# Optimization experiments

Hardware: AMD Instinct MI355X
Metric: run time of the kernel (lower is better)

The kernel has to match this reference:

```python
import jax, jax.numpy as jnp
import numpy as np

ATOM_VOC = 128
PAD = 0

def setup_inputs() -> dict:
    key = jax.random.key(0)
    ks = jax.random.split(key, 12)
    b, l, d_model, nhead, apo = 8, 256, 512, 16, 128
    atoms = jax.random.randint(ks[0], (b, l), 0, ATOM_VOC)
    chirals = jax.random.randint(ks[1], (b, l), 0, 4)
    coordinates = jax.random.normal(ks[2], (b, l, 3), dtype=jnp.float32)
    bonds = jax.random.randint(ks[3], (b, l, l), 0, 32)
    atype_emb = jax.random.normal(ks[4], (ATOM_VOC, d_model), jnp.float32).at[PAD].set(0.0)
    chiral_emb = jax.random.normal(ks[5], (4, d_model), jnp.float32).at[PAD].set(0.0)
    apair_w_tab = jax.random.normal(ks[6], (ATOM_VOC * ATOM_VOC, apo), jnp.float32)
    apair_b_tab = jax.random.normal(ks[7], (ATOM_VOC * ATOM_VOC, apo), jnp.float32)
    means = jnp.zeros((apo,), jnp.float32)
    stds = jnp.ones((apo,), jnp.float32)
    bond_emb = jax.random.normal(ks[8], (32, nhead), jnp.float32).at[PAD].set(0.0)
    lin_w = jax.random.normal(ks[9], (apo, nhead), jnp.float32) / np.sqrt(apo)
    lin_b = jax.random.normal(ks[10], (nhead,), jnp.float32)
    return dict(atoms=atoms, chirals=chirals, coordinates=coordinates, bonds=bonds,
                atype_emb=atype_emb, chiral_emb=chiral_emb, apair_w_tab=apair_w_tab,
                apair_b_tab=apair_b_tab, means=means, stds=stds, bond_emb=bond_emb,
                lin_w=lin_w, lin_b=lin_b)

def _safe_dist(coordinates):
    # pairwise distances [b,l,l]; safe-sqrt so grad at 0 distance is 0 (diagonal)
    diff = coordinates[:, None, :, :] - coordinates[:, :, None, :]
    s = jnp.sum(diff * diff, axis=-1)
    return jnp.where(s > 0, jnp.sqrt(jnp.where(s > 0, s, 1.0)), 0.0)

def reference(atoms, chirals, coordinates, bonds, atype_emb, chiral_emb,
              apair_w_tab, apair_b_tab, means, stds, bond_emb, lin_w, lin_b):
    # atoms_emb: [l, b, d_model]
    atoms_emb = (atype_emb[atoms] + chiral_emb[chirals]).transpose(1, 0, 2)
    dist = _safe_dist(coordinates)                      # [b,l,l]
    pair_idx = atoms[:, None, :] * ATOM_VOC + atoms[:, :, None]  # [b,l,l]
    ap = apair_w_tab[pair_idx] * dist[..., None] + apair_b_tab[pair_idx]  # [b,l,l,apo]
    std = jnp.abs(stds) + 1e-5
    gauss = jnp.exp(-0.5 * ((ap - means) / std) ** 2) / (np.sqrt(2.0 * np.pi) * std)
    apairs = jnp.einsum('bijk,kh->bijh', gauss, lin_w) + lin_b + bond_emb[bonds]
    pad_mask = (atoms == PAD)[:, None, :, None]         # mask over key/column dim
    apairs = jnp.where(pad_mask, -jnp.inf, apairs)
    return atoms_emb, apairs.transpose(0, 3, 1, 2)      # [b,nhead,l,l]
```

## Files before the change

kernel.cpp:

```cpp
#include <hip/hip_runtime.h>
#include <hip/hip_fp16.h>
#include <math.h>
#include <stdint.h>

#define B 8
#define L 256
#define DM 512
#define NH 16
#define APO 128
#define VOC 128
#define EMB (L * B * DM)

typedef __attribute__((ext_vector_type(8))) _Float16 half8v;
typedef __attribute__((ext_vector_type(4))) float float4v;

#define WSB_BOFF   1024
#define ORD_BOFF   9216
#define PACK_BOFF  24576
#define PACK_BYTES (128 * 128 * 256)
#define WS_NEED    ((size_t)PACK_BOFF + (size_t)PACK_BYTES)

__device__ __forceinline__ void g2lds16(const void* g, void* l) {
    __builtin_amdgcn_global_load_lds(
        (const __attribute__((address_space(1))) unsigned int*)g,
        (__attribute__((address_space(3))) unsigned int*)l, 16, 0, 0);
}

__global__ __launch_bounds__(256) void pack_kernel(const float* __restrict__ wtab,
                                                   const float* __restrict__ btab,
                                                   const float* __restrict__ means,
                                                   const float* __restrict__ stds,
                                                   const float* __restrict__ lin_w,
                                                   const int* __restrict__ atoms,
                                                   float* __restrict__ ws) {
    const float beta = sqrtf(0.5f * 1.4426950408889634f);
    const float gscale = 0.3989422804014327f;
    int t = threadIdx.x;

    if (blockIdx.x == 0) {
        unsigned short* wsB = (unsigned short*)((char*)ws + WSB_BOFF);
        for (int idx = t; idx < 4 * 64 * 8; idx += 256) {
            int p = idx >> 9;
            int lane = (idx >> 3) & 63;
            int e = idx & 7;
            int k = p * 32 + ((lane >> 4) << 3) + e;
            int h = lane & 15;
            float sigma = fabsf(stds[k]) + 1e-5f;
            float v = lin_w[k * NH + h] * (gscale / sigma);
            __half hv = __float2half(v);
            wsB[idx] = *reinterpret_cast<unsigned short*>(&hv);
        }
        __shared__ int hist[128];
        if (t < 128) hist[t] = 0;
        __syncthreads();
        for (int vb = t; vb < 2048; vb += 256)
            atomicAdd(&hist[atoms[vb] & 127], 1);
        __syncthreads();
        __shared__ int offs[128];
        if (t == 0) {
            int acc = 0;
            for (int bkt = 0; bkt < 128; ++bkt) { offs[bkt] = acc; acc += hist[bkt]; }
        }
        __syncthreads();
        int* order = (int*)((char*)ws + ORD_BOFF);
        for (int vb = t; vb < 2048; vb += 256) {
            int a = atoms[vb] & 127;
            int pos = atomicAdd(&offs[a], 1);
            order[pos] = vb;
        }
    }

    int idx = blockIdx.x * 256 + t;
    int r = idx >> 4;
    int a_i = r >> 7, a_j = r & 127;
    int U = idx & 15;
    int k0 = U * 8;
    size_t src = ((size_t)a_j * VOC + a_i) * APO + k0;
    const float4* w4p = (const float4*)(wtab + src);
    const float4* b4p = (const float4*)(btab + src);
    float4 w0 = w4p[0], w1 = w4p[1], b0 = b4p[0], b1 = b4p[1];
    float wq[8], bq[8];
    #pragma unroll
    for (int e = 0; e < 8; ++e) {
        int k = k0 + e;
        float sigma = fabsf(stds[k]) + 1e-5f;
        float ia = beta / sigma;
        float wvv = ((e < 4) ? ((const float*)&w0)[e] : ((const float*)&w1)[e - 4]) * ia;
        float bvv = (((e < 4) ? ((const float*)&b0)[e] : ((const float*)&b1)[e - 4])
                     - means[k]) * ia;
        wq[e] = wvv; bq[e] = bvv;
    }
    int wlo = 0, whi = 0, blo = 0, bhi = 0;
    wlo = __builtin_amdgcn_cvt_pk_fp8_f32(wq[0], wq[1], wlo, 0);
    wlo = __builtin_amdgcn_cvt_pk_fp8_f32(wq[2], wq[3], wlo, 1);
    whi = __builtin_amdgcn_cvt_pk_fp8_f32(wq[4], wq[5], whi, 0);
    whi = __builtin_amdgcn_cvt_pk_fp8_f32(wq[6], wq[7], whi, 1);
    blo = __builtin_amdgcn_cvt_pk_fp8_f32(bq[0], bq[1], blo, 0);
    blo = __builtin_amdgcn_cvt_pk_fp8_f32(bq[2], bq[3], blo, 1);
    bhi = __builtin_amdgcn_cvt_pk_fp8_f32(bq[4], bq[5], bhi, 0);
    bhi = __builtin_amdgcn_cvt_pk_fp8_f32(bq[6], bq[7], bhi, 1);
    int pu = U ^ (a_j & 15);
    uint4 o;
    o.x = (unsigned)wlo; o.y = (unsigned)whi;
    o.z = (unsigned)blo; o.w = (unsigned)bhi;
    *(uint4*)((char*)ws + PACK_BOFF + (size_t)r * 256 + (size_t)pu * 16) = o;
}

__global__ __launch_bounds__(256, 5) void pair_fused(const int* __restrict__ atoms,
                                                     const int* __restrict__ chirals,
                                                     const float* __restrict__ coords,
                                                     const int* __restrict__ bonds,
                                                     const float* __restrict__ atype,
                                                     const float* __restrict__ chiral,
                                                     const float* __restrict__ bond_emb,
                                                     const float* __restrict__ lin_b,
                                                     const float* __restrict__ ws,
                                                     float* __restrict__ out) {
    __shared__ __align__(16) char stage[32 * 1024];

    int t = threadIdx.x;
    int p = blockIdx.x;
    const int* order = (const int*)((const char*)ws + ORD_BOFF);
    int vb = order[(p & 7) * 256 + (p >> 3)];
    int bi = vb >> 8, i = vb & 255;
    int w = t >> 6, l = t & 63;

    int a_i = atoms[bi * L + i];
    int av = atoms[bi * L + t];

    float cix = coords[((size_t)bi * L + i) * 3 + 0];
    float ciy = coords[((size_t)bi * L + i) * 3 + 1];
    float ciz = coords[((size_t)bi * L + i) * 3 + 2];
    float cjx = coords[((size_t)bi * L + t) * 3 + 0];
    float cjy = coords[((size_t)bi * L + t) * 3 + 1];
    float cjz = coords[((size_t)bi * L + t) * 3 + 2];
    float dx = cjx - cix, dy = cjy - ciy, dz = cjz - ciz;
    float s2 = dx * dx + dy * dy + dz * dz;
    float d = (s2 > 0.0f) ? sqrtf(s2) : 0.0f;
    int dbits = __float_as_int(d);

    half8v bfrag[4];
    {
        const uint4* wb = (const uint4*)((const char*)ws + WSB_BOFF);
        #pragma unroll
        for (int pp = 0; pp < 4; ++pp) {
            uint4 r = wb[pp * 64 + l];
            bfrag[pp] = *reinterpret_cast<half8v*>(&r);
        }
    }

    int m = l >> 4;
    float dval[4];
    int base[4], ax[4];
    #pragma unroll
    for (int q = 0; q < 4; ++q) {
        int idx4 = (q * 16 + (l & 15)) * 4;
        int a = __builtin_amdgcn_ds_bpermute(idx4, av);
        dval[q] = __int_as_float(__builtin_amdgcn_ds_bpermute(idx4, dbits));
        base[q] = a * 256;
        ax[q] = a & 15;
    }

    float4v acc[4];
    #pragma unroll
    for (int q = 0; q < 4; ++q) { float4v z = {0, 0, 0, 0}; acc[q] = z; }

    const char* pkbi = (const char*)ws + PACK_BOFF + (size_t)a_i * 32768;

    #pragma unroll
    for (int it = 0; it < 8; ++it) {
        size_t off = (size_t)(w * 32 + it * 4) * 256 + (size_t)l * 16;
        g2lds16(pkbi + off, stage + off);
    }
    asm volatile("s_waitcnt vmcnt(0)" ::: "memory");
    __syncthreads();

    if (t < 128) {
        int a = atoms[bi * L + i];
        int c = chirals[bi * L + i];
        const float4* va = (const float4*)(atype + (size_t)a * DM);
        const float4* vc = (const float4*)(chiral + (size_t)c * DM);
        float4 x = va[t], y = vc[t];
        x.x += y.x; x.y += y.y; x.z += y.z; x.w += y.w;
        ((float4*)(out + ((size_t)i * B + bi) * DM))[t] = x;
    }

    #pragma unroll
    for (int rr = 0; rr < 4; ++rr) {
        #pragma unroll
        for (int q = 0; q < 4; ++q) {
            int un = (rr * 4 + m) ^ ax[q];
            uint4 u = *(const uint4*)(stage + base[q] + (un << 4));
            auto w01 = __builtin_amdgcn_cvt_pk_f32_fp8((int)u.x, 0);
            auto w23 = __builtin_amdgcn_cvt_pk_f32_fp8((int)u.x, 1);
            auto w45 = __builtin_amdgcn_cvt_pk_f32_fp8((int)u.y, 0);
            auto w67 = __builtin_amdgcn_cvt_pk_f32_fp8((int)u.y, 1);
            auto b01 = __builtin_amdgcn_cvt_pk_f32_fp8((int)u.z, 0);
            auto b23 = __builtin_amdgcn_cvt_pk_f32_fp8((int)u.z, 1);
            auto b45 = __builtin_amdgcn_cvt_pk_f32_fp8((int)u.w, 0);
            auto b67 = __builtin_amdgcn_cvt_pk_f32_fp8((int)u.w, 1);
            float dq = dval[q];
            float t0 = fmaf(w01[0], dq, b01[0]);
            float t1 = fmaf(w01[1], dq, b01[1]);
            float t2 = fmaf(w23[0], dq, b23[0]);
            float t3 = fmaf(w23[1], dq, b23[1]);
            float t4 = fmaf(w45[0], dq, b45[0]);
            float t5 = fmaf(w45[1], dq, b45[1]);
            float t6 = fmaf(w67[0], dq, b67[0]);
            float t7 = fmaf(w67[1], dq, b67[1]);
            float g0 = __builtin_amdgcn_exp2f(-(t0 * t0));
            float g1 = __builtin_amdgcn_exp2f(-(t1 * t1));
            float g2 = __builtin_amdgcn_exp2f(-(t2 * t2));
            float g3 = __builtin_amdgcn_exp2f(-(t3 * t3));
            float g4 = __builtin_amdgcn_exp2f(-(t4 * t4));
            float g5 = __builtin_amdgcn_exp2f(-(t5 * t5));
            float g6 = __builtin_amdgcn_exp2f(-(t6 * t6));
            float g7 = __builtin_amdgcn_exp2f(-(t7 * t7));
            auto p0 = __builtin_amdgcn_cvt_pkrtz(g0, g1);
            auto p1 = __builtin_amdgcn_cvt_pkrtz(g2, g3);
            auto p2 = __builtin_amdgcn_cvt_pkrtz(g4, g5);
            auto p3 = __builtin_amdgcn_cvt_pkrtz(g6, g7);
            uint4 au;
            au.x = *reinterpret_cast<unsigned*>(&p0);
            au.y = *reinterpret_cast<unsigned*>(&p1);
            au.z = *reinterpret_cast<unsigned*>(&p2);
            au.w = *reinterpret_cast<unsigned*>(&p3);
            half8v af = *reinterpret_cast<half8v*>(&au);
            acc[q] = __builtin_amdgcn_mfma_f32_16x16x32_f16(af, bfrag[rr],
                                                            acc[q], 0, 0, 0);
        }
    }

    asm volatile("s_waitcnt lgkmcnt(0)" ::: "memory");
    __syncthreads();

    int a_j = atoms[bi * L + t];
    int bvd = bonds[(((size_t)bi * L) + i) * L + t];
    float beh[NH];
    {
        const float4* ber = (const float4*)(bond_emb + (size_t)bvd * NH);
        #pragma unroll
        for (int u = 0; u < 4; ++u) {
            float4 v4 = ber[u];
            beh[u * 4 + 0] = v4.x; beh[u * 4 + 1] = v4.y;
            beh[u * 4 + 2] = v4.z; beh[u * 4 + 3] = v4.w;
        }
    }
    float* cbuf = (float*)(stage + (size_t)w * 4352);
    {
        int h = l & 15, jg = l >> 4;
        #pragma unroll
        for (int q = 0; q < 4; ++q)
            *(float4v*)(cbuf + h * 68 + q * 16 + jg * 4) = acc[q];
    }
    asm volatile("s_waitcnt lgkmcnt(0)" ::: "memory");
    __builtin_amdgcn_sched_barrier(0);

    size_t obase = (((size_t)bi * NH) * L + i) * L + t;
    float ninf = __uint_as_float(0xff7f0000u);
    bool pad = (a_j == 0);
    #pragma unroll
    for (int h = 0; h < NH; ++h) {
        float v = cbuf[h * 68 + l] + lin_b[h] + beh[h];
        out[(size_t)EMB + obase + (size_t)h * L * L] = pad ? ninf : v;
    }
}

extern "C" void kernel_launch(void* const* d_in, const int* in_sizes, int n_in,
                              void* d_out, int out_size, void* d_ws, size_t ws_size,
                              hipStream_t stream) {
    const int*   atoms    = (const int*)d_in[0];
    const int*   chirals  = (const int*)d_in[1];
    const float* coords   = (const float*)d_in[2];
    const int*   bonds    = (const int*)d_in[3];
    const float* atype    = (const float*)d_in[4];
    const float* chiral   = (const float*)d_in[5];
    const float* wtab     = (const float*)d_in[6];
    const float* btab     = (const float*)d_in[7];
    const float* means    = (const float*)d_in[8];
    const float* stds     = (const float*)d_in[9];
    const float* bond_emb = (const float*)d_in[10];
    const float* lin_w    = (const float*)d_in[11];
    const float* lin_b    = (const float*)d_in[12];
    float* out = (float*)d_out;
    float* ws  = (float*)d_ws;

    pack_kernel<<<1024, 256, 0, stream>>>(wtab, btab, means, stds, lin_w, atoms, ws);
    pair_fused<<<B * L, 256, 0, stream>>>(atoms, chirals, coords, bonds,
                                          atype, chiral, bond_emb, lin_b, ws, out);
}
```

Baseline: 32.62 us.

## Process two query rows per block, reusing staged pack table when atoms match

Each block now handles two (batch,row) pairs taken from consecutive slots of the sort order, which halves the grid to 1024 blocks. The per-row packed weight/bias table is staged into LDS once and only reloaded when the second row's atom type differs, so rows sorted by atom type can share the stage. Launch bounds drop to 4 waves per SIMD to make room for the doubled accumulators and indices. The cost is more registers per thread, lower occupancy, and an extra sync-and-reload path when the atom types differ.

```diff
diff --git a/kernel.cpp b/kernel.cpp
--- a/kernel.cpp
+++ b/kernel.cpp
@@ -106,7 +106,7 @@
     *(uint4*)((char*)ws + PACK_BOFF + (size_t)r * 256 + (size_t)pu * 16) = o;
 }
 
-__global__ __launch_bounds__(256, 5) void pair_fused(const int* __restrict__ atoms,
+__global__ __launch_bounds__(256, 4) void pair_fused(const int* __restrict__ atoms,
                                                      const int* __restrict__ chirals,
                                                      const float* __restrict__ coords,
                                                      const int* __restrict__ bonds,
@@ -121,23 +121,46 @@
     int t = threadIdx.x;
     int p = blockIdx.x;
     const int* order = (const int*)((const char*)ws + ORD_BOFF);
-    int vb = order[(p & 7) * 256 + (p >> 3)];
-    int bi = vb >> 8, i = vb & 255;
+    int slot = (p & 7) * 256 + (p >> 3) * 2;
+    int vb0 = order[slot], vb1 = order[slot + 1];
+    int bi0 = vb0 >> 8, i0 = vb0 & 255;
+    int bi1 = vb1 >> 8, i1 = vb1 & 255;
     int w = t >> 6, l = t & 63;
-
-    int a_i = atoms[bi * L + i];
-    int av = atoms[bi * L + t];
-
-    float cix = coords[((size_t)bi * L + i) * 3 + 0];
-    float ciy = coords[((size_t)bi * L + i) * 3 + 1];
-    float ciz = coords[((size_t)bi * L + i) * 3 + 2];
-    float cjx = coords[((size_t)bi * L + t) * 3 + 0];
-    float cjy = coords[((size_t)bi * L + t) * 3 + 1];
-    float cjz = coords[((size_t)bi * L + t) * 3 + 2];
-    float dx = cjx - cix, dy = cjy - ciy, dz = cjz - ciz;
-    float s2 = dx * dx + dy * dy + dz * dz;
-    float d = (s2 > 0.0f) ? sqrtf(s2) : 0.0f;
-    int dbits = __float_as_int(d);
+    int m = l >> 4;
+
+    int a_i0 = atoms[vb0];
+    int a_i1 = atoms[vb1];
+    int av0 = atoms[bi0 * L + t];
+    int av1 = atoms[bi1 * L + t];
+
+    const char* pk0 = (const char*)ws + PACK_BOFF + (size_t)a_i0 * 32768;
+    #pragma unroll
+    for (int it = 0; it < 8; ++it) {
+        size_t off = (size_t)(w * 32 + it * 4) * 256 + (size_t)l * 16;
+        g2lds16(pk0 + off, stage + off);
+    }
+
+    float d0, d1;
+    {
+        float cix = coords[((size_t)bi0 * L + i0) * 3 + 0];
+        float ciy = coords[((size_t)bi0 * L + i0) * 3 + 1];
+        float ciz = coords[((size_t)bi0 * L + i0) * 3 + 2];
+        float cjx = coords[((size_t)bi0 * L + t) * 3 + 0];
+        float cjy = coords[((size_t)bi0 * L + t) * 3 + 1];
+        float cjz = coords[((size_t)bi0 * L + t) * 3 + 2];
+        float dx = cjx - cix, dy = cjy - ciy, dz = cjz - ciz;
+        float s2 = dx * dx + dy * dy + dz * dz;
+        d0 = (s2 > 0.0f) ? sqrtf(s2) : 0.0f;
+        cix = coords[((size_t)bi1 * L + i1) * 3 + 0];
+        ciy = coords[((size_t)bi1 * L + i1) * 3 + 1];
+        ciz = coords[((size_t)bi1 * L + i1) * 3 + 2];
+        cjx = coords[((size_t)bi1 * L + t) * 3 + 0];
+        cjy = coords[((size_t)bi1 * L + t) * 3 + 1];
+        cjz = coords[((size_t)bi1 * L + t) * 3 + 2];
+        dx = cjx - cix; dy = cjy - ciy; dz = cjz - ciz;
+        s2 = dx * dx + dy * dy + dz * dz;
+        d1 = (s2 > 0.0f) ? sqrtf(s2) : 0.0f;
+    }
 
     half8v bfrag[4];
     {
@@ -149,121 +172,151 @@
         }
     }
 
-    int m = l >> 4;
-    float dval[4];
-    int base[4], ax[4];
+    float dval0[4], dval1[4];
+    int base0[4], ax0[4], base1[4], ax1[4];
+    {
+        int db0 = __float_as_int(d0), db1 = __float_as_int(d1);
+        #pragma unroll
+        for (int q = 0; q < 4; ++q) {
+            int idx4 = (q * 16 + (l & 15)) * 4;
+            int a0 = __builtin_amdgcn_ds_bpermute(idx4, av0);
+            int a1 = __builtin_amdgcn_ds_bpermute(idx4, av1);
+            dval0[q] = __int_as_float(__builtin_amdgcn_ds_bpermute(idx4, db0));
+            dval1[q] = __int_as_float(__builtin_amdgcn_ds_bpermute(idx4, db1));
+            base0[q] = a0 * 256; ax0[q] = a0 & 15;
+            base1[q] = a1 * 256; ax1[q] = a1 & 15;
+        }
+    }
+
+    float4v acc0[4], acc1[4];
     #pragma unroll
     for (int q = 0; q < 4; ++q) {
-        int idx4 = (q * 16 + (l & 15)) * 4;
-        int a = __builtin_amdgcn_ds_bpermute(idx4, av);
-        dval[q] = __int_as_float(__builtin_amdgcn_ds_bpermute(idx4, dbits));
-        base[q] = a * 256;
-        ax[q] = a & 15;
-    }
-
-    float4v acc[4];
-    #pragma unroll
-    for (int q = 0; q < 4; ++q) { float4v z = {0, 0, 0, 0}; acc[q] = z; }
-
-    const char* pkbi = (const char*)ws + PACK_BOFF + (size_t)a_i * 32768;
-
-    #pragma unroll
-    for (int it = 0; it < 8; ++it) {
-        size_t off = (size_t)(w * 32 + it * 4) * 256 + (size_t)l * 16;
-        g2lds16(pkbi + off, stage + off);
-    }
+        float4v z = {0, 0, 0, 0};
+        acc0[q] = z; acc1[q] = z;
+    }
+
+#define COMPUTE(ACC, DVAL, BASE, AX)                                            \
+    {                                                                           \
+        _Pragma("unroll")                                                       \
+        for (int rr = 0; rr < 4; ++rr) {                                        \
+            _Pragma("unroll")                                                   \
+            for (int q = 0; q < 4; ++q) {                                       \
+                int un = (rr * 4 + m) ^ AX[q];                                  \
+                uint4 u = *(const uint4*)(stage + BASE[q] + (un << 4));         \
+                auto w01 = __builtin_amdgcn_cvt_pk_f32_fp8((int)u.x, 0);        \
+                auto w23 = __builtin_amdgcn_cvt_pk_f32_fp8((int)u.x, 1);        \
+                auto w45 = __builtin_amdgcn_cvt_pk_f32_fp8((int)u.y, 0);        \
+                auto w67 = __builtin_amdgcn_cvt_pk_f32_fp8((int)u.y, 1);        \
+                auto b01 = __builtin_amdgcn_cvt_pk_f32_fp8((int)u.z, 0);        \
+                auto b23 = __builtin_amdgcn_cvt_pk_f32_fp8((int)u.z, 1);        \
+                auto b45 = __builtin_amdgcn_cvt_pk_f32_fp8((int)u.w, 0);        \
+                auto b67 = __builtin_amdgcn_cvt_pk_f32_fp8((int)u.w, 1);        \
+                float dq = DVAL[q];                                             \
+                float t0 = fmaf(w01[0], dq, b01[0]);                            \
+                float t1 = fmaf(w01[1], dq, b01[1]);                            \
+                float t2 = fmaf(w23[0], dq, b23[0]);                            \
+                float t3 = fmaf(w23[1], dq, b23[1]);                            \
+                float t4 = fmaf(w45[0], dq, b45[0]);                            \
+                float t5 = fmaf(w45[1], dq, b45[1]);                            \
+                float t6 = fmaf(w67[0], dq, b67[0]);                            \
+                float t7 = fmaf(w67[1], dq, b67[1]);                            \
+                float g0 = __builtin_amdgcn_exp2f(-(t0 * t0));                  \
+                float g1 = __builtin_amdgcn_exp2f(-(t1 * t1));                  \
+                float g2 = __builtin_amdgcn_exp2f(-(t2 * t2));                  \
+                float g3 = __builtin_amdgcn_exp2f(-(t3 * t3));                  \
+                float g4 = __builtin_amdgcn_exp2f(-(t4 * t4));                  \
+                float g5 = __builtin_amdgcn_exp2f(-(t5 * t5));                  \
+                float g6 = __builtin_amdgcn_exp2f(-(t6 * t6));                  \
+                float g7 = __builtin_amdgcn_exp2f(-(t7 * t7));                  \
+                auto p0 = __builtin_amdgcn_cvt_pkrtz(g0, g1);                   \
+                auto p1 = __builtin_amdgcn_cvt_pkrtz(g2, g3);                   \
+                auto p2 = __builtin_amdgcn_cvt_pkrtz(g4, g5);                   \
+                auto p3 = __builtin_amdgcn_cvt_pkrtz(g6, g7);                   \
+                uint4 au;                                                       \
+                au.x = *reinterpret_cast<unsigned*>(&p0);                       \
+                au.y = *reinterpret_cast<unsigned*>(&p1);                       \
+                au.z = *reinterpret_cast<unsigned*>(&p2);                       \
+                au.w = *reinterpret_cast<unsigned*>(&p3);                       \
+                half8v af = *reinterpret_cast<half8v*>(&au);                    \
+                ACC[q] = __builtin_amdgcn_mfma_f32_16x16x32_f16(af, bfrag[rr],  \
+                                                                ACC[q], 0, 0, 0);\
+            }                                                                   \
+        }                                                                       \
+    }
+
+#define EPILOGUE(ACC, BI, I)                                                    \
+    {                                                                           \
+        int a_j = atoms[(BI) * L + t];                                          \
+        int bvd = bonds[(((size_t)(BI) * L) + (I)) * L + t];                    \
+        float beh[NH];                                                          \
+        const float4* ber = (const float4*)(bond_emb + (size_t)bvd * NH);       \
+        _Pragma("unroll")                                                       \
+        for (int u = 0; u < 4; ++u) {                                           \
+            float4 v4 = ber[u];                                                 \
+            beh[u * 4 + 0] = v4.x; beh[u * 4 + 1] = v4.y;                       \
+            beh[u * 4 + 2] = v4.z; beh[u * 4 + 3] = v4.w;                       \
+        }                                                                       \
+        float* cbuf = (float*)(stage + (size_t)w * 4352);                       \
+        {                                                                       \
+            int h = l & 15, jg = l >> 4;                                        \
+            _Pragma("unroll")                                                   \
+            for (int q = 0; q < 4; ++q)                                         \
+                *(float4v*)(cbuf + h * 68 + q * 16 + jg * 4) = ACC[q];          \
+        }                                                                       \
+        asm volatile("s_waitcnt lgkmcnt(0)" ::: "memory");                      \
+        __builtin_amdgcn_sched_barrier(0);                                      \
+        size_t obase = (((size_t)(BI) * NH) * L + (I)) * L + t;                 \
+        float ninf = __uint_as_float(0xff7f0000u);                              \
+        bool pad = (a_j == 0);                                                  \
+        _Pragma("unroll")                                                       \
+        for (int h = 0; h < NH; ++h) {                                          \
+            float v = cbuf[h * 68 + l] + lin_b[h] + beh[h];                     \
+            out[(size_t)EMB + obase + (size_t)h * L * L] = pad ? ninf : v;      \
+        }                                                                       \
+    }
+
     asm volatile("s_waitcnt vmcnt(0)" ::: "memory");
     __syncthreads();
 
     if (t < 128) {
-        int a = atoms[bi * L + i];
-        int c = chirals[bi * L + i];
+        int a = atoms[vb0], c = chirals[vb0];
         const float4* va = (const float4*)(atype + (size_t)a * DM);
         const float4* vc = (const float4*)(chiral + (size_t)c * DM);
         float4 x = va[t], y = vc[t];
         x.x += y.x; x.y += y.y; x.z += y.z; x.w += y.w;
-        ((float4*)(out + ((size_t)i * B + bi) * DM))[t] = x;
-    }
-
-    #pragma unroll
-    for (int rr = 0; rr < 4; ++rr) {
+        ((float4*)(out + ((size_t)i0 * B + bi0) * DM))[t] = x;
+        a = atoms[vb1]; c = chirals[vb1];
+        va = (const float4*)(atype + (size_t)a * DM);
+        vc = (const float4*)(chiral + (size_t)c * DM);
+        float4 x1 = va[t], y1 = vc[t];
+        x1.x += y1.x; x1.y += y1.y; x1.z += y1.z; x1.w += y1.w;
+        ((float4*)(out + ((size_t)i1 * B + bi1) * DM))[t] = x1;
+    }
+
+    COMPUTE(acc0, dval0, base0, ax0)
+
+    if (a_i1 != a_i0) {
+        asm volatile("s_waitcnt lgkmcnt(0)" ::: "memory");
+        __syncthreads();
+        const char* pk1 = (const char*)ws + PACK_BOFF + (size_t)a_i1 * 32768;
         #pragma unroll
-        for (int q = 0; q < 4; ++q) {
-            int un = (rr * 4 + m) ^ ax[q];
-            uint4 u = *(const uint4*)(stage + base[q] + (un << 4));
-            auto w01 = __builtin_amdgcn_cvt_pk_f32_fp8((int)u.x, 0);
-            auto w23 = __builtin_amdgcn_cvt_pk_f32_fp8((int)u.x, 1);
-            auto w45 = __builtin_amdgcn_cvt_pk_f32_fp8((int)u.y, 0);
-            auto w67 = __builtin_amdgcn_cvt_pk_f32_fp8((int)u.y, 1);
-            auto b01 = __builtin_amdgcn_cvt_pk_f32_fp8((int)u.z, 0);
-            auto b23 = __builtin_amdgcn_cvt_pk_f32_fp8((int)u.z, 1);
-            auto b45 = __builtin_amdgcn_cvt_pk_f32_fp8((int)u.w, 0);
-            auto b67 = __builtin_amdgcn_cvt_pk_f32_fp8((int)u.w, 1);
-            float dq = dval[q];
-            float t0 = fmaf(w01[0], dq, b01[0]);
-            float t1 = fmaf(w01[1], dq, b01[1]);
-            float t2 = fmaf(w23[0], dq, b23[0]);
-            float t3 = fmaf(w23[1], dq, b23[1]);
-            float t4 = fmaf(w45[0], dq, b45[0]);
-            float t5 = fmaf(w45[1], dq, b45[1]);
-            float t6 = fmaf(w67[0], dq, b67[0]);
-            float t7 = fmaf(w67[1], dq, b67[1]);
-            float g0 = __builtin_amdgcn_exp2f(-(t0 * t0));
-            float g1 = __builtin_amdgcn_exp2f(-(t1 * t1));
-            float g2 = __builtin_amdgcn_exp2f(-(t2 * t2));
-            float g3 = __builtin_amdgcn_exp2f(-(t3 * t3));
-            float g4 = __builtin_amdgcn_exp2f(-(t4 * t4));
-            float g5 = __builtin_amdgcn_exp2f(-(t5 * t5));
-            float g6 = __builtin_amdgcn_exp2f(-(t6 * t6));
-            float g7 = __builtin_amdgcn_exp2f(-(t7 * t7));
-            auto p0 = __builtin_amdgcn_cvt_pkrtz(g0, g1);
-            auto p1 = __builtin_amdgcn_cvt_pkrtz(g2, g3);
-            auto p2 = __builtin_amdgcn_cvt_pkrtz(g4, g5);
-            auto p3 = __builtin_amdgcn_cvt_pkrtz(g6, g7);
-            uint4 au;
-            au.x = *reinterpret_cast<unsigned*>(&p0);
-            au.y = *reinterpret_cast<unsigned*>(&p1);
-            au.z = *reinterpret_cast<unsigned*>(&p2);
-            au.w = *reinterpret_cast<unsigned*>(&p3);
-            half8v af = *reinterpret_cast<half8v*>(&au);
-            acc[q] = __builtin_amdgcn_mfma_f32_16x16x32_f16(af, bfrag[rr],
-                                                            acc[q], 0, 0, 0);
-        }
-    }
+        for (int it = 0; it < 8; ++it) {
+            size_t off = (size_t)(w * 32 + it * 4) * 256 + (size_t)l * 16;
+            g2lds16(pk1 + off, stage + off);
+        }
+        asm volatile("s_waitcnt vmcnt(0)" ::: "memory");
+        __syncthreads();
+    }
+
+    COMPUTE(acc1, dval1, base1, ax1)
 
     asm volatile("s_waitcnt lgkmcnt(0)" ::: "memory");
     __syncthreads();
 
-    int a_j = atoms[bi * L + t];
-    int bvd = bonds[(((size_t)bi * L) + i) * L + t];
-    float beh[NH];
-    {
-        const float4* ber = (const float4*)(bond_emb + (size_t)bvd * NH);
-        #pragma unroll
-        for (int u = 0; u < 4; ++u) {
-            float4 v4 = ber[u];
-            beh[u * 4 + 0] = v4.x; beh[u * 4 + 1] = v4.y;
-            beh[u * 4 + 2] = v4.z; beh[u * 4 + 3] = v4.w;
-        }
-    }
-    float* cbuf = (float*)(stage + (size_t)w * 4352);
-    {
-        int h = l & 15, jg = l >> 4;
-        #pragma unroll
-        for (int q = 0; q < 4; ++q)
-            *(float4v*)(cbuf + h * 68 + q * 16 + jg * 4) = acc[q];
-    }
-    asm volatile("s_waitcnt lgkmcnt(0)" ::: "memory");
-    __builtin_amdgcn_sched_barrier(0);
-
-    size_t obase = (((size_t)bi * NH) * L + i) * L + t;
-    float ninf = __uint_as_float(0xff7f0000u);
-    bool pad = (a_j == 0);
-    #pragma unroll
-    for (int h = 0; h < NH; ++h) {
-        float v = cbuf[h * 68 + l] + lin_b[h] + beh[h];
-        out[(size_t)EMB + obase + (size_t)h * L * L] = pad ? ninf : v;
-    }
+    EPILOGUE(acc0, bi0, i0)
+    EPILOGUE(acc1, bi1, i1)
+#undef COMPUTE
+#undef EPILOGUE
 }
 
 extern "C" void kernel_launch(void* const* d_in, const int* in_sizes, int n_in,
@@ -286,6 +339,6 @@
     float* ws  = (float*)d_ws;
 
     pack_kernel<<<1024, 256, 0, stream>>>(wtab, btab, means, stds, lin_w, atoms, ws);
-    pair_fused<<<B * L, 256, 0, stream>>>(atoms, chirals, coords, bonds,
-                                          atype, chiral, bond_emb, lin_b, ws, out);
+    pair_fused<<<1024, 256, 0, stream>>>(atoms, chirals, coords, bonds,
+                                         atype, chiral, bond_emb, lin_b, ws, out);
 }
```

New measurement: 34.06 us. +4.4%, slower.
